# Kernel optimization log

Hardware: AMD Instinct MI355X
Metric: run time of the kernel (lower is better)

## Reference

```python
import jax, jax.numpy as jnp
import numpy as np

B, S, C = 2, 2048, 1536
HQ, HKV = 16, 4
DQK, DV = 128, 96
MAX_POS = 2048
CLIP = 5.0
EPS = 1e-5


def layer_norm(x, g, b):
    mu = jnp.mean(x, axis=-1, keepdims=True)
    var = jnp.mean(jnp.square(x - mu), axis=-1, keepdims=True)
    return (x - mu) * jax.lax.rsqrt(var + EPS) * g + b


def rms_bn(x, g, ms):
    # eval-mode EMA RMS batch-norm: per-channel running mean-square `ms`
    return x * jax.lax.rsqrt(ms + EPS) * g


def rope(x):
    # x: [B, S, H, C] with C even
    c = x.shape[-1]
    nf = c // 2
    s = x.shape[1]
    positions = jnp.arange(s, dtype=x.dtype)
    lin = jnp.arange(nf, dtype=x.dtype)
    end = max(MAX_POS - nf + 1.0, 1.0)
    geom = jnp.exp(jnp.linspace(0.0, jnp.log(jnp.asarray(end, dtype=x.dtype)), nf))
    inv_freq = 1.0 / (lin + geom)
    theta = positions[:, None] * inv_freq          # [S, nf]
    theta = jnp.repeat(theta, 2, axis=-1)[:, None, :]  # [S, 1, C]
    x_rot = jnp.stack([-x[..., 1::2], x[..., ::2]], axis=-1).reshape(x.shape)
    return x * jnp.cos(theta) + x_rot * jnp.sin(theta)


def setup_inputs() -> dict:
    key = jax.random.key(0)
    ks = jax.random.split(key, 8)
    d = {
        'x': jax.random.normal(ks[0], (B, S, C), dtype=jnp.float32),
        'bn1_g': jnp.ones((C,), jnp.float32),
        'bn1_ms': jnp.ones((C,), jnp.float32),
        'Wq': jax.random.normal(ks[1], (C, HQ * DQK), jnp.float32) * 0.02,
        'Wk': jax.random.normal(ks[2], (C, HKV * DQK), jnp.float32) * 0.02,
        'Wv': jax.random.normal(ks[3], (C, HKV * DV), jnp.float32) * 0.02,
        'qn_g': jnp.ones((DQK,), jnp.float32), 'qn_b': jnp.zeros((DQK,), jnp.float32),
        'kn_g': jnp.ones((DQK,), jnp.float32), 'kn_b': jnp.zeros((DQK,), jnp.float32),
        'vn_g': jnp.ones((DV,), jnp.float32), 'vn_b': jnp.zeros((DV,), jnp.float32),
        'Wo': jax.random.normal(ks[4], (HQ * DV, C), jnp.float32) * 0.02,
        'bo': jnp.zeros((C,), jnp.float32),
        'bn2_g': jnp.ones((C,), jnp.float32),
        'bn2_ms': jnp.ones((C,), jnp.float32),
    }
    return d


def reference(x, bn1_g, bn1_ms, Wq, Wk, Wv, qn_g, qn_b, kn_g, kn_b, vn_g, vn_b, Wo, bo, bn2_g, bn2_ms):
    rep = HQ // HKV
    h = rms_bn(x, bn1_g, bn1_ms)                       # [B,S,C]
    q = (h @ Wq).reshape(B, S, HQ, DQK)
    k = (h @ Wk).reshape(B, S, HKV, DQK)
    v = (h @ Wv).reshape(B, S, HKV, DV)
    q = layer_norm(q, qn_g, qn_b)
    k = layer_norm(k, kn_g, kn_b)
    v = layer_norm(v, vn_g, vn_b)
    q = rope(q)
    k = rope(k)
    # torch .repeat(1,1,rep,1) tiles head axis: [h0..hkv-1] * rep
    k = jnp.tile(k, (1, 1, rep, 1))                    # [B,S,HQ,DQK]
    v = jnp.tile(v, (1, 1, rep, 1))                    # [B,S,HQ,DV]
    logits = jnp.einsum('bshc,bShc->bhsS', q, k) / (DQK ** 0.5)
    logits = jnp.tanh(logits / CLIP) * CLIP
    attn = jax.nn.softmax(logits, axis=-1)
    y = jnp.einsum('bhsS,bShc->bshc', attn, v)         # [B,S,HQ,DV]
    y = y.reshape(B, S, HQ * DV)
    y = y @ Wo + bo
    y = rms_bn(y, bn2_g, bn2_ms)
    return y
```

## Files before the change

kernel.cpp:

```cpp
#include <hip/hip_runtime.h>
#include <hip/hip_bf16.h>
#include <math.h>

typedef __hip_bfloat16 bf16;
typedef __attribute__((ext_vector_type(8))) short short8;
typedef __attribute__((ext_vector_type(4))) short short4s;
typedef __attribute__((ext_vector_type(4))) float f32x4;

constexpr int Bb=2, Ss=2048, Cc=1536, HQn=16, HKVn=4, Dqk=128, Dv=96;
constexpr int NR   = Bb*Ss;
constexpr int NQKV = HQn*Dqk + HKVn*Dqk + HKVn*Dv;
constexpr int COL_K = HQn*Dqk;
constexpr int COL_V = COL_K + HKVn*Dqk;
constexpr int NY   = HQn*Dv;
constexpr float EPSf=1e-5f, CLIPf=5.0f;
constexpr float LOG2E = 1.44269504089f;

__device__ __forceinline__ float s2f(short s) {
    unsigned u = ((unsigned)(unsigned short)s) << 16;
    return __builtin_bit_cast(float, u);
}
__device__ __forceinline__ short f2s(float v) {
    bf16 b = __float2bfloat16(v);
    return __builtin_bit_cast(short, b);
}
__device__ __forceinline__ bool is_bf(const void* tagp) {
    return ((*(const unsigned*)tagp) & 0xFFFFu) != 0u;
}
__device__ __forceinline__ float ldd(const void* p, size_t i, bool bf) {
    return bf ? s2f(((const short*)p)[i]) : ((const float*)p)[i];
}
__device__ __forceinline__ void gll16(const void* src, void* lds) {
    __builtin_amdgcn_global_load_lds(
        (const __attribute__((address_space(1))) void*)src,
        (__attribute__((address_space(3))) void*)lds, 16, 0, 0);
}

__global__ __launch_bounds__(256) void k_pre(const void* g1, const void* ms1,
        const void* bo, const void* g2, const void* ms2,
        float* __restrict__ ascale, float* __restrict__ ebias,
        float* __restrict__ escale, float2* __restrict__ tab) {
    bool bf = is_bf(ms1);
    int idx = blockIdx.x*256 + threadIdx.x;
    if (idx < Cc) {
        ascale[idx] = rsqrtf(ldd(ms1,idx,bf) + EPSf) * ldd(g1,idx,bf);
        ebias[idx]  = ldd(bo,idx,bf);
        escale[idx] = rsqrtf(ldd(ms2,idx,bf) + EPSf) * ldd(g2,idx,bf);
    }
    if (idx < Ss*64) {
        int s = idx >> 6, f = idx & 63;
        float geom = expf((float)f * (logf(1985.0f) * (1.0f/63.0f)));
        float invf = 1.0f / ((float)f + geom);
        float th = (float)s * invf;
        tab[idx] = make_float2(cosf(th), sinf(th));
    }
}

__global__ __launch_bounds__(256) void k_bn1(const void* __restrict__ x,
        short* __restrict__ h, const void* tagp) {
    bool bf = is_bf(tagp);
    size_t i8 = (size_t)(blockIdx.x*256 + threadIdx.x) * 8;
    if (i8 >= (size_t)NR*Cc) return;
    if (bf) {
        *(short8*)(h + i8) = *(const short8*)((const short*)x + i8);
    } else {
        const float* xf = (const float*)x + i8;
        short8 o;
        #pragma unroll
        for (int j=0;j<8;++j) o[j] = f2s(xf[j]);
        *(short8*)(h + i8) = o;
    }
}

__global__ __launch_bounds__(256) void k_trw(const void* __restrict__ Wq,
        const void* __restrict__ Wk, const void* __restrict__ Wv,
        const void* __restrict__ Wo, short* __restrict__ WT,
        const float* __restrict__ ascale, const void* tagp) {
    __shared__ short tile[32][33];
    bool bf = is_bf(tagp);
    int gt = blockIdx.x*32;
    int k0 = blockIdx.y*32;
    const void* W; int N, nl;
    bool doscale = true;
    if      (gt < 2048) { W = Wq; N = 2048; nl = gt; }
    else if (gt < 2560) { W = Wk; N = 512;  nl = gt - 2048; }
    else if (gt < 2944) { W = Wv; N = 384;  nl = gt - 2560; }
    else                { W = Wo; N = 1536; nl = gt - 2944; doscale = false; }
    int t = threadIdx.x, c = t & 31;
    #pragma unroll
    for (int r8=0; r8<32; r8+=8) {
        int r = r8 + (t>>5);
        float sc = doscale ? ascale[k0+r] : 1.0f;
        tile[r][c] = f2s(ldd(W, (size_t)(k0+r)*N + nl + c, bf) * sc);
    }
    __syncthreads();
    #pragma unroll
    for (int r8=0; r8<32; r8+=8) {
        int r = r8 + (t>>5);
        WT[(size_t)(gt + r)*Cc + k0 + c] = tile[c][r];
    }
}

__global__ __launch_bounds__(256) void k_gemm(const short* __restrict__ A,
        const short* __restrict__ BT, void* __restrict__ Cout,
        int M, int N, int K,
        const float* __restrict__ ebias, const float* __restrict__ escale,
        int epi, const void* tagp) {
    __shared__ short As[128*32];
    __shared__ short Bs[128*32];
    const int t = threadIdx.x;
    const int w = t >> 6, lane = t & 63;
    const int l15 = lane & 15, quad = lane >> 4;
    const int wm = (w>>1)*64, wn = (w&1)*64;
    const int m0 = blockIdx.y*128, n0 = blockIdx.x*128;
    const int c0 = lane >> 2;
    const int koff = (lane & 3) * 8;

    f32x4 acc[4][4];
    #pragma unroll
    for (int i=0;i<4;++i)
        #pragma unroll
        for (int j=0;j<4;++j) acc[i][j] = (f32x4){0.f,0.f,0.f,0.f};

    for (int k0 = 0; k0 < K; k0 += 32) {
        __syncthreads();
        #pragma unroll
        for (int c=0; c<2; ++c) {
            int rA = w*32 + c*16;
            const short* ga = A  + (size_t)(m0 + rA + c0)*K + k0 + koff;
            const short* gb = BT + (size_t)(n0 + rA + c0)*K + k0 + koff;
            gll16(ga, &As[rA*32]);
            gll16(gb, &Bs[rA*32]);
        }
        __syncthreads();
        short8 af[4], bfr[4];
        #pragma unroll
        for (int mt=0; mt<4; ++mt)
            af[mt] = *(const short8*)&As[(wm + mt*16 + l15)*32 + quad*8];
        #pragma unroll
        for (int nt=0; nt<4; ++nt)
            bfr[nt] = *(const short8*)&Bs[(wn + nt*16 + l15)*32 + quad*8];
        #pragma unroll
        for (int mt=0; mt<4; ++mt)
            #pragma unroll
            for (int nt=0; nt<4; ++nt)
                acc[mt][nt] = __builtin_amdgcn_mfma_f32_16x16x32_bf16(
                    af[mt], bfr[nt], acc[mt][nt], 0, 0, 0);
    }

    const bool outf32 = epi && !is_bf(tagp);
    #pragma unroll
    for (int mt=0; mt<4; ++mt) {
        #pragma unroll
        for (int nt=0; nt<4; ++nt) {
            int col = n0 + wn + nt*16 + l15;
            float eb = epi ? ebias[col]  : 0.f;
            float es = epi ? escale[col] : 1.f;
            #pragma unroll
            for (int reg=0; reg<4; ++reg) {
                int row = m0 + wm + mt*16 + quad*4 + reg;
                float v = acc[mt][nt][reg];
                if (epi) v = (v + eb) * es;
                if (outf32) ((float*)Cout)[(size_t)row*N + col] = v;
                else        ((short*)Cout)[(size_t)row*N + col] = f2s(v);
            }
        }
    }
}

__global__ __launch_bounds__(512, 2) void k_gemm256(const short* __restrict__ A,
        const short* __restrict__ BT, short* __restrict__ Cout,
        int M, int Npad, int Nout, int K) {
    __shared__ __align__(16) short As[2][256*64];
    __shared__ __align__(16) short Bs[2][256*64];
    const int t = threadIdx.x;
    const int w = t >> 6, lane = t & 63;
    const int wm = w >> 2, wn = w & 3;
    const int l15 = lane & 15, quad = lane >> 4;
    const int xr = (l15 & 7) * 16;

    const int nwg = gridDim.x, cpx = nwg >> 3;
    const int swz = (blockIdx.x & 7)*cpx + (blockIdx.x >> 3);
    const int ntx = Npad >> 8;
    const int n0 = (swz % ntx) << 8, m0 = (swz / ntx) << 8;

    const int rA0 = (w*64 + lane) >> 3;
    const int csw = (((lane & 7) * 16) ^ ((rA0 & 7) << 4));
    const short* Abase = A  + (size_t)(m0 + rA0)*K;
    const short* Bbase = BT + (size_t)(n0 + rA0)*K;

    f32x4 acc[8][4];
    #pragma unroll
    for (int i=0;i<8;++i)
        #pragma unroll
        for (int j=0;j<4;++j) acc[i][j] = (f32x4){0.f,0.f,0.f,0.f};

    auto stage = [&](int kt, int pb) {
        const char* as = (const char*)Abase + (size_t)kt*128 + csw;
        const char* bs = (const char*)Bbase + (size_t)kt*128 + csw;
        char* AD = (char*)&As[pb][0] + w*1024;
        char* BD = (char*)&Bs[pb][0] + w*1024;
        const size_t RADV = (size_t)64*K*2;
        #pragma unroll
        for (int it=0; it<4; ++it) {
            gll16(as + it*RADV, AD + it*8192);
            gll16(bs + it*RADV, BD + it*8192);
        }
    };

    stage(0, 0);
    asm volatile("s_waitcnt vmcnt(0)" ::: "memory");
    __builtin_amdgcn_s_barrier();

    const int NT = K >> 6;
    for (int kt = 0; kt < NT; ++kt) {
        const int cur = kt & 1;
        const bool pf = (kt+1 < NT);
        const char* AsB = (const char*)&As[cur][0];
        const char* BsB = (const char*)&Bs[cur][0];
        #pragma unroll
        for (int ph=0; ph<4; ++ph) {
            if (ph == 0 && pf) stage(kt+1, cur^1);
            const int mg = ph >> 1, ks = ph & 1;
            short8 af[4], bf_[4];
            #pragma unroll
            for (int i=0; i<4; ++i) {
                int rowa = wm*128 + (mg*4+i)*16 + l15;
                af[i] = *(const short8*)(AsB + rowa*128 + ((ks*64 + quad*16) ^ xr));
                int rowb = wn*64 + i*16 + l15;
                bf_[i] = *(const short8*)(BsB + rowb*128 + ((ks*64 + quad*16) ^ xr));
            }
            __builtin_amdgcn_s_barrier();
            asm volatile("s_waitcnt lgkmcnt(0)" ::: "memory");
            __builtin_amdgcn_sched_barrier(0);
            __builtin_amdgcn_s_setprio(1);
            #pragma unroll
            for (int i=0; i<4; ++i)
                #pragma unroll
                for (int j=0; j<4; ++j)
                    acc[mg*4+i][j] = __builtin_amdgcn_mfma_f32_16x16x32_bf16(
                        af[i], bf_[j], acc[mg*4+i][j], 0, 0, 0);
            __builtin_amdgcn_s_setprio(0);
            if (ph == 3 && pf) asm volatile("s_waitcnt vmcnt(0)" ::: "memory");
            __builtin_amdgcn_s_barrier();
        }
    }

    #pragma unroll
    for (int mt=0; mt<8; ++mt) {
        #pragma unroll
        for (int nt=0; nt<4; ++nt) {
            int col = n0 + wn*64 + nt*16 + l15;
            if (col < Nout) {
                #pragma unroll
                for (int reg=0; reg<4; ++reg) {
                    int row = m0 + wm*128 + mt*16 + quad*4 + reg;
                    Cout[(size_t)row*Nout + col] = f2s(acc[mt][nt][reg]);
                }
            }
        }
    }
}

__global__ __launch_bounds__(256) void k_ln(short* __restrict__ qkvb,
        const float2* __restrict__ tab,
        const void* qg, const void* qb_, const void* kg, const void* kb_,
        const void* vg, const void* vb_, const void* tagp) {
    bool bf = is_bf(tagp);
    int R = blockIdx.x*4 + (threadIdx.x>>6);
    int lane = threadIdx.x & 63;
    int hidx = R % 24, bs = R / 24, s = bs % Ss;
    const void *g, *bia; int coff, D, dorope;
    if (hidx < 16)      { coff = hidx*Dqk;              D = Dqk; g = qg; bia = qb_; dorope = 1; }
    else if (hidx < 20) { coff = COL_K + (hidx-16)*Dqk; D = Dqk; g = kg; bia = kb_; dorope = 1; }
    else                { coff = COL_V + (hidx-20)*Dv;  D = Dv;  g = vg; bia = vb_; dorope = 0; }
    short* p = qkvb + (size_t)bs*NQKV + coff;
    int d0 = lane*2;
    bool act = d0 < D;
    float v0 = 0.f, v1 = 0.f;
    if (act) { v0 = s2f(p[d0]); v1 = s2f(p[d0+1]); }
    float sum = v0 + v1;
    #pragma unroll
    for (int m=1; m<64; m<<=1) sum += __shfl_xor(sum, m);
    float mu = sum / (float)D;
    float c0 = act ? v0-mu : 0.f, c1 = act ? v1-mu : 0.f;
    float sq = c0*c0 + c1*c1;
    #pragma unroll
    for (int m=1; m<64; m<<=1) sq += __shfl_xor(sq, m);
    float r = rsqrtf(sq/(float)D + EPSf);
    if (act) {
        float y0 = c0*r*ldd(g,d0,bf)   + ldd(bia,d0,bf);
        float y1 = c1*r*ldd(g,d0+1,bf) + ldd(bia,d0+1,bf);
        if (dorope) {
            float2 cs = tab[s*64 + lane];
            float t0 = y0*cs.x - y1*cs.y;
            y1 = y1*cs.x + y0*cs.y;
            y0 = t0;
        }
        p[d0] = f2s(y0); p[d0+1] = f2s(y1);
    }
}

__global__ __launch_bounds__(256) void k_trv(const short* __restrict__ qkvb,
        short* __restrict__ vT) {
    __shared__ short tile[32][33];
    int bs0 = blockIdx.x*32;
    int dg0 = blockIdx.y*32;
    int t = threadIdx.x, c = t & 31;
    #pragma unroll
    for (int r8=0; r8<32; r8+=8) {
        int r = r8 + (t>>5);
        tile[r][c] = qkvb[(size_t)(bs0+r)*NQKV + COL_V + dg0 + c];
    }
    __syncthreads();
    int b = bs0 >> 11, s0 = bs0 & 2047;
    int s = s0 + c;
    int sp = (s & ~63) + ((s>>5)&1)*32 + ((s>>2)&3)*8 + ((s>>4)&1)*4 + (s&3);
    #pragma unroll
    for (int r8=0; r8<32; r8+=8) {
        int r = r8 + (t>>5);
        vT[((size_t)(b*384 + dg0 + r))*Ss + sp] = tile[c][r];
    }
}

__global__ __launch_bounds__(512, 4) void k_attn(const short* __restrict__ qkvb,
        const short* __restrict__ vT, short* __restrict__ Yb) {
    __shared__ __align__(16) short smem[2*64*128 + 2*96*64];
    auto Ks  = (short(*)[64*128])smem;
    auto VTs = (short(*)[96*64])(smem + 2*64*128);
    const int wg = blockIdx.x;
    const int xcd = wg & 7, idx = wg >> 3;
    const int b = xcd >> 2, kvh = xcd & 3;
    const int qb = idx >> 2, hsub = idx & 3;
    const int hq = hsub*4 + kvh;
    const int q0 = qb*128;
    const int t = threadIdx.x;
    const int w = t >> 6, lane = t & 63;
    const int qw = w & 3, half = w >> 2;
    const int l15 = lane & 15, quad = lane >> 4;
    const int xr = (l15 & 7) * 16;
    const float ctan = 2.0f * (0.0883883476f / CLIPf) * LOG2E;
    const float c2   = -2.0f * CLIPf * LOG2E;

    const short* Kb = qkvb + ((size_t)b*Ss)*NQKV + COL_K + kvh*Dqk;
    const short* Vb = vT + ((size_t)(b*HKVn + kvh)*Dv)*Ss;

    const int rK = 4*w + (lane>>4);
    const char* kq0 = (const char*)Kb + (size_t)rK*NQKV*2
                    + (((lane&15)*16) ^ ((rK&7)*16));
    const int dv0 = 8*w + (lane>>3);
    const char* vq0 = (const char*)Vb + (size_t)dv0*Ss*2
                    + (((lane&7)*16) ^ ((dv0&7)*16));
    const size_t KADV = (size_t)64*NQKV*2;
    const size_t KOFF2 = (size_t)32*NQKV*2;
    const size_t VOFF2 = (size_t)64*Ss*2;

    auto issue_stage = [&](int pb) {
        char* KD = (char*)&Ks[pb][0];
        char* VD = (char*)&VTs[pb][0];
        gll16(kq0,         KD + w*1024);
        gll16(kq0 + KOFF2, KD + (w+8)*1024);
        gll16(vq0,         VD + w*1024);
        if (w < 4) gll16(vq0 + VOFF2, VD + (w+8)*1024);
        kq0 += KADV; vq0 += 128;
    };

    issue_stage(0);

    short8 qf[2][4];
    #pragma unroll
    for (int qt=0; qt<2; ++qt) {
        const short* qp = qkvb + (size_t)(b*Ss + q0 + qw*32 + qt*16 + l15)*NQKV + hq*Dqk;
        #pragma unroll
        for (int ds=0; ds<4; ++ds) qf[qt][ds] = *(const short8*)(qp + ds*32 + quad*8);
    }

    f32x4 oacc[2][6];
    #pragma unroll
    for (int qt=0; qt<2; ++qt)
        #pragma unroll
        for (int nt=0; nt<6; ++nt) oacc[qt][nt] = (f32x4){0.f,0.f,0.f,0.f};
    float lsum[2] = {0.f, 0.f};

    int p = 0;
    constexpr int NCH = Ss/64;
    for (int kc = 0; kc < NCH; ++kc) {
        __syncthreads();
        if (kc+1 < NCH) issue_stage(p^1);

        const char* KsB  = (const char*)&Ks[p][0];
        const char* VTsB = (const char*)&VTs[p][0];

        short8 pa[2];
        #pragma unroll
        for (int kt=0; kt<2; ++kt) {
            const int r = (half*2 + kt)*16 + l15;
            const char* krow = KsB + r*256;
            short8 kf[4];
            #pragma unroll
            for (int ds=0; ds<4; ++ds)
                kf[ds] = *(const short8*)(krow + ((ds*64 + quad*16) ^ xr));
            f32x4 s0 = (f32x4){0.f,0.f,0.f,0.f}, s1 = (f32x4){0.f,0.f,0.f,0.f};
            __builtin_amdgcn_s_setprio(1);
            #pragma unroll
            for (int ds=0; ds<4; ++ds) {
                s0 = __builtin_amdgcn_mfma_f32_16x16x32_bf16(kf[ds], qf[0][ds], s0, 0, 0, 0);
                s1 = __builtin_amdgcn_mfma_f32_16x16x32_bf16(kf[ds], qf[1][ds], s1, 0, 0, 0);
            }
            __builtin_amdgcn_s_setprio(0);
            #pragma unroll
            for (int j=0; j<4; ++j) {
                float u0 = __builtin_amdgcn_exp2f(s0[j] * ctan);
                float p0 = __builtin_amdgcn_exp2f(c2 * __builtin_amdgcn_rcpf(u0 + 1.0f));
                pa[0][kt*4+j] = f2s(p0); lsum[0] += p0;
                float u1 = __builtin_amdgcn_exp2f(s1[j] * ctan);
                float p1 = __builtin_amdgcn_exp2f(c2 * __builtin_amdgcn_rcpf(u1 + 1.0f));
                pa[1][kt*4+j] = f2s(p1); lsum[1] += p1;
            }
        }

        __builtin_amdgcn_s_setprio(1);
        #pragma unroll
        for (int nt=0; nt<6; ++nt) {
            const int dvrow = nt*16 + l15;
            short8 vf = *(const short8*)(VTsB + dvrow*128 + ((half*64 + quad*16) ^ xr));
            oacc[0][nt] = __builtin_amdgcn_mfma_f32_16x16x32_bf16(pa[0], vf, oacc[0][nt], 0, 0, 0);
            oacc[1][nt] = __builtin_amdgcn_mfma_f32_16x16x32_bf16(pa[1], vf, oacc[1][nt], 0, 0, 0);
        }
        __builtin_amdgcn_s_setprio(0);
        p ^= 1;
    }

    __syncthreads();
    float* red = (float*)smem;
    const int rbase = (qw*64 + lane)*52;
    if (half == 1) {
        #pragma unroll
        for (int qt=0; qt<2; ++qt)
            #pragma unroll
            for (int nt=0; nt<6; ++nt)
                *(f32x4*)&red[rbase + (qt*6+nt)*4] = oacc[qt][nt];
        red[rbase+48] = lsum[0];
        red[rbase+49] = lsum[1];
    }
    __syncthreads();
    if (half == 0) {
        #pragma unroll
        for (int qt=0; qt<2; ++qt)
            #pragma unroll
            for (int nt=0; nt<6; ++nt) {
                f32x4 o = *(const f32x4*)&red[rbase + (qt*6+nt)*4];
                #pragma unroll
                for (int j=0;j<4;++j) oacc[qt][nt][j] += o[j];
            }
        lsum[0] += red[rbase+48];
        lsum[1] += red[rbase+49];

        float lred[2];
        #pragma unroll
        for (int qt=0; qt<2; ++qt) {
            float l = lsum[qt];
            l += __shfl_xor(l, 16);
            l += __shfl_xor(l, 32);
            lred[qt] = l;
        }
        #pragma unroll
        for (int qt=0; qt<2; ++qt) {
            float rinv[4];
            #pragma unroll
            for (int reg=0; reg<4; ++reg)
                rinv[reg] = __builtin_amdgcn_rcpf(__shfl(lred[qt], quad*4 + reg, 16));
            #pragma unroll
            for (int nt=0; nt<6; ++nt)
                #pragma unroll
                for (int reg=0; reg<4; ++reg) {
                    int row = q0 + qw*32 + qt*16 + quad*4 + reg;
                    Yb[(size_t)(b*Ss + row)*NY + hq*Dv + nt*16 + l15] =
                        f2s(oacc[qt][nt][reg] * rinv[reg]);
                }
        }
    }
}

extern "C" void kernel_launch(void* const* d_in, const int* in_sizes, int n_in,
                              void* d_out, int out_size, void* d_ws, size_t ws_size,
                              hipStream_t stream) {
    const void* x     = d_in[0];
    const void* bn1g  = d_in[1];
    const void* bn1ms = d_in[2];
    const void* Wq    = d_in[3];
    const void* Wk    = d_in[4];
    const void* Wv    = d_in[5];
    const void* qng   = d_in[6];
    const void* qnb   = d_in[7];
    const void* kng   = d_in[8];
    const void* knb   = d_in[9];
    const void* vng   = d_in[10];
    const void* vnb   = d_in[11];
    const void* Wo    = d_in[12];
    const void* bo    = d_in[13];
    const void* bn2g  = d_in[14];
    const void* bn2ms = d_in[15];

    char* wsb = (char*)d_ws;
    float*  ascale = (float*)(wsb);
    float*  ebias  = (float*)(wsb + 6144);
    float*  escale = (float*)(wsb + 12288);
    float2* tab    = (float2*)(wsb + 18432);
    short*  h      = (short*)(wsb + 1067520);
    short*  WT     = (short*)(wsb + 13650432);
    short*  qkv    = (short*)(wsb + 27412992);
    short*  vT     = (short*)(wsb + 51530240);
    short*  y      = (short*)(wsb + 54675968);
    short*  WoT    = WT + (size_t)NQKV*Cc;

    k_pre<<<512, 256, 0, stream>>>(bn1g, bn1ms, bo, bn2g, bn2ms,
                                   ascale, ebias, escale, tab);

    const short* Agemm;
    if (in_sizes && in_sizes[0] == (int)((size_t)NR*Cc*2)) {
        Agemm = (const short*)x;
    } else {
        k_bn1<<<(NR*Cc/8 + 255)/256, 256, 0, stream>>>(x, h, bn1ms);
        Agemm = h;
    }

    k_trw<<<dim3(4480/32, Cc/32), 256, 0, stream>>>(Wq, Wk, Wv, Wo, WT, ascale, bn1ms);

    k_gemm256<<<dim3(192), 512, 0, stream>>>(Agemm, WT, qkv, NR, 3072, NQKV, Cc);

    k_ln<<<NR*24/4, 256, 0, stream>>>(qkv, tab, qng, qnb, kng, knb, vng, vnb, bn1ms);
    k_trv<<<dim3(NR/32, 384/32), 256, 0, stream>>>(qkv, vT);

    k_attn<<<512, 512, 0, stream>>>(qkv, vT, y);

    k_gemm<<<dim3(Cc/128, NR/128), 256, 0, stream>>>(
        y, WoT, d_out, NR, Cc, NY, ebias, escale, 1, bn1ms);
}
```

Baseline: 342.5 us.

## Load K and V fragments directly from global memory instead of LDS staging

Removes the double-buffered LDS staging of K and V tiles (global-to-LDS loads, swizzle, and per-chunk barriers) in the attention kernel. Each lane now reads its K and V MFMA fragments straight from global memory (relying on L1/L2 caching), and LDS is kept only for the final cross-half reduction. This drops the block-wide synchronisation and LDS traffic, but every wave issues its own redundant global loads, which adds cache pressure and leaves load latency without explicit prefetch.

```diff
diff --git a/kernel.cpp b/kernel.cpp
--- a/kernel.cpp
+++ b/kernel.cpp
@@ -325,9 +325,7 @@
 
 __global__ __launch_bounds__(512, 4) void k_attn(const short* __restrict__ qkvb,
         const short* __restrict__ vT, short* __restrict__ Yb) {
-    __shared__ __align__(16) short smem[2*64*128 + 2*96*64];
-    auto Ks  = (short(*)[64*128])smem;
-    auto VTs = (short(*)[96*64])(smem + 2*64*128);
+    __shared__ float red[256*52];
     const int wg = blockIdx.x;
     const int xcd = wg & 7, idx = wg >> 3;
     const int b = xcd >> 2, kvh = xcd & 3;
@@ -338,35 +336,9 @@
     const int w = t >> 6, lane = t & 63;
     const int qw = w & 3, half = w >> 2;
     const int l15 = lane & 15, quad = lane >> 4;
-    const int xr = (l15 & 7) * 16;
     const float ctan = 2.0f * (0.0883883476f / CLIPf) * LOG2E;
     const float c2   = -2.0f * CLIPf * LOG2E;
 
-    const short* Kb = qkvb + ((size_t)b*Ss)*NQKV + COL_K + kvh*Dqk;
-    const short* Vb = vT + ((size_t)(b*HKVn + kvh)*Dv)*Ss;
-
-    const int rK = 4*w + (lane>>4);
-    const char* kq0 = (const char*)Kb + (size_t)rK*NQKV*2
-                    + (((lane&15)*16) ^ ((rK&7)*16));
-    const int dv0 = 8*w + (lane>>3);
-    const char* vq0 = (const char*)Vb + (size_t)dv0*Ss*2
-                    + (((lane&7)*16) ^ ((dv0&7)*16));
-    const size_t KADV = (size_t)64*NQKV*2;
-    const size_t KOFF2 = (size_t)32*NQKV*2;
-    const size_t VOFF2 = (size_t)64*Ss*2;
-
-    auto issue_stage = [&](int pb) {
-        char* KD = (char*)&Ks[pb][0];
-        char* VD = (char*)&VTs[pb][0];
-        gll16(kq0,         KD + w*1024);
-        gll16(kq0 + KOFF2, KD + (w+8)*1024);
-        gll16(vq0,         VD + w*1024);
-        if (w < 4) gll16(vq0 + VOFF2, VD + (w+8)*1024);
-        kq0 += KADV; vq0 += 128;
-    };
-
-    issue_stage(0);
-
     short8 qf[2][4];
     #pragma unroll
     for (int qt=0; qt<2; ++qt) {
@@ -382,24 +354,26 @@
         for (int nt=0; nt<6; ++nt) oacc[qt][nt] = (f32x4){0.f,0.f,0.f,0.f};
     float lsum[2] = {0.f, 0.f};
 
-    int p = 0;
+    const short* kp = qkvb + (size_t)(b*Ss + half*32 + l15)*NQKV + COL_K + kvh*Dqk + quad*8;
+    const short* vp = vT + ((size_t)(b*HKVn + kvh)*Dv + l15)*Ss + half*32 + quad*8;
+
     constexpr int NCH = Ss/64;
     for (int kc = 0; kc < NCH; ++kc) {
-        __syncthreads();
-        if (kc+1 < NCH) issue_stage(p^1);
-
-        const char* KsB  = (const char*)&Ks[p][0];
-        const char* VTsB = (const char*)&VTs[p][0];
+        const short* kpc = kp + (size_t)kc*64*NQKV;
+        const short* vpc = vp + kc*64;
+
+        short8 vf[6];
+        #pragma unroll
+        for (int nt=0; nt<6; ++nt)
+            vf[nt] = *(const short8*)(vpc + (size_t)nt*16*Ss);
 
         short8 pa[2];
         #pragma unroll
         for (int kt=0; kt<2; ++kt) {
-            const int r = (half*2 + kt)*16 + l15;
-            const char* krow = KsB + r*256;
             short8 kf[4];
             #pragma unroll
             for (int ds=0; ds<4; ++ds)
-                kf[ds] = *(const short8*)(krow + ((ds*64 + quad*16) ^ xr));
+                kf[ds] = *(const short8*)(kpc + (size_t)kt*16*NQKV + ds*32);
             f32x4 s0 = (f32x4){0.f,0.f,0.f,0.f}, s1 = (f32x4){0.f,0.f,0.f,0.f};
             __builtin_amdgcn_s_setprio(1);
             #pragma unroll
@@ -422,17 +396,13 @@
         __builtin_amdgcn_s_setprio(1);
         #pragma unroll
         for (int nt=0; nt<6; ++nt) {
-            const int dvrow = nt*16 + l15;
-            short8 vf = *(const short8*)(VTsB + dvrow*128 + ((half*64 + quad*16) ^ xr));
-            oacc[0][nt] = __builtin_amdgcn_mfma_f32_16x16x32_bf16(pa[0], vf, oacc[0][nt], 0, 0, 0);
-            oacc[1][nt] = __builtin_amdgcn_mfma_f32_16x16x32_bf16(pa[1], vf, oacc[1][nt], 0, 0, 0);
+            oacc[0][nt] = __builtin_amdgcn_mfma_f32_16x16x32_bf16(pa[0], vf[nt], oacc[0][nt], 0, 0, 0);
+            oacc[1][nt] = __builtin_amdgcn_mfma_f32_16x16x32_bf16(pa[1], vf[nt], oacc[1][nt], 0, 0, 0);
         }
         __builtin_amdgcn_s_setprio(0);
-        p ^= 1;
     }
 
     __syncthreads();
-    float* red = (float*)smem;
     const int rbase = (qw*64 + lane)*52;
     if (half == 1) {
         #pragma unroll
```

Result: slower. 577.3 us (+68.6%).
